# Kernel optimization log

Hardware: AMD Instinct MI355X
Metric: run time of the kernel (lower is better)

The kernel has to match this reference:

```python
import jax, jax.numpy as jnp
import numpy as np

N = 50000      # nodes
E = 600000     # directed edges (before self-loops)
IN, HID, OUT = 512, 128, 40
EPS_BN = 1e-5
DROP_P = 0.5   # hardcoded in forward via BernoulliDropout(0.5)

# BinActive: sign() forward, straight-through estimator backward (|x|<=1 gate)
@jax.custom_vjp
def binactive(x):
    return jnp.sign(x)

def _ba_fwd(x):
    return jnp.sign(x), x

def _ba_bwd(x, g):
    return (g * (jnp.abs(x) <= 1.0).astype(g.dtype),)

binactive.defvjp(_ba_fwd, _ba_bwd)


def setup_inputs() -> dict:
    key = jax.random.key(0)
    ks = jax.random.split(key, 8)
    x = jax.random.normal(ks[0], (N, IN), dtype=jnp.float32)
    edge_index = jax.random.randint(ks[1], (2, E), 0, N, dtype=jnp.int64)
    w0 = jax.random.normal(ks[2], (IN, HID), dtype=jnp.float32) * 0.05
    b0 = jnp.zeros((HID,), jnp.float32)
    w1 = jax.random.normal(ks[3], (HID, HID), dtype=jnp.float32) * 0.05
    b1 = jnp.zeros((HID,), jnp.float32)
    w2 = jax.random.normal(ks[4], (HID, OUT), dtype=jnp.float32) * 0.05
    b2 = jnp.zeros((OUT,), jnp.float32)
    return {"x": x, "edge_index": edge_index,
            "w0": w0, "b0": b0, "w1": w1, "b1": b1, "w2": w2, "b2": b2}


def _gcn_norm(edge_index):
    # add self-loops, compute symmetric normalization deg^-1/2 A deg^-1/2
    loops = jnp.arange(N, dtype=edge_index.dtype)
    row = jnp.concatenate([edge_index[0], loops])  # destinations
    col = jnp.concatenate([edge_index[1], loops])  # sources
    deg = jax.ops.segment_sum(jnp.ones_like(row, dtype=jnp.float32), row, num_segments=N)
    dinv = jnp.where(deg > 0, deg ** -0.5, 0.0)
    norm = dinv[row] * dinv[col]                   # [E+N]
    return row, col, norm


def _gcn_conv(x, w, b, row, col, norm):
    # binarized weight: sign(w) scaled by mean(|w|) (XNOR-style)
    wb = binactive(w) * jnp.mean(jnp.abs(w))
    h = x @ wb                                     # [N, out]
    msg = h[col] * norm[:, None]                   # gather + scale
    agg = jax.ops.segment_sum(msg, row, num_segments=N)
    return agg + b


def reference(x, edge_index, w0, b0, w1, b1, w2, b2):
    # BatchNorm1d(affine=False), training-mode batch stats over nodes
    mean = jnp.mean(x, axis=0)
    var = jnp.var(x, axis=0)
    h = (x - mean) / jnp.sqrt(var + EPS_BN)

    row, col, norm = _gcn_norm(edge_index)
    dkey = jax.random.key(42)
    weights = [(w0, b0), (w1, b1), (w2, b2)]
    n_layers = len(weights)
    for i, (w, b) in enumerate(weights):
        h = binactive(h)
        h = _gcn_conv(h, w, b, row, col, norm)
        if i != n_layers - 1:  # BernoulliDropout(0.5)
            mask = jax.random.bernoulli(jax.random.fold_in(dkey, i), 1.0 - DROP_P, h.shape)
            h = h * mask.astype(h.dtype) * (1.0 / (1.0 - DROP_P))
    return jax.nn.log_softmax(h, axis=1)
```

## Files before the change

kernel.cpp:

```cpp
#include <hip/hip_runtime.h>
#include <stdint.h>
#include <stddef.h>

#define NN 50000
#define NE 600000
#define DI 512
#define DH 128
#define DO 40
#define MTOT (NN * DH)
#define NBLK ((NN + 255) / 256)

using int4v = __attribute__((ext_vector_type(4))) int;

__host__ __device__ inline uint32_t rotl32(uint32_t v, int d) {
  return (v << d) | (v >> (32 - d));
}

__host__ __device__ inline void threefry2x32(uint32_t k0, uint32_t k1,
                                             uint32_t c0, uint32_t c1,
                                             uint32_t* o0, uint32_t* o1) {
  uint32_t ks0 = k0, ks1 = k1, ks2 = k0 ^ k1 ^ 0x1BD11BDAu;
  uint32_t x0 = c0 + ks0, x1 = c1 + ks1;
  const int R0[4] = {13, 15, 26, 6};
  const int R1[4] = {17, 29, 16, 24};
#define TF_R4(R) { x0 += x1; x1 = rotl32(x1, R[0]); x1 ^= x0; \
                   x0 += x1; x1 = rotl32(x1, R[1]); x1 ^= x0; \
                   x0 += x1; x1 = rotl32(x1, R[2]); x1 ^= x0; \
                   x0 += x1; x1 = rotl32(x1, R[3]); x1 ^= x0; }
  TF_R4(R0); x0 += ks1; x1 += ks2 + 1u;
  TF_R4(R1); x0 += ks2; x1 += ks0 + 2u;
  TF_R4(R0); x0 += ks0; x1 += ks1 + 3u;
  TF_R4(R1); x0 += ks1; x1 += ks2 + 4u;
  TF_R4(R0); x0 += ks2; x1 += ks0 + 5u;
#undef TF_R4
  *o0 = x0; *o1 = x1;
}

__global__ void colsum_kernel(const float* __restrict__ x,
                              double* __restrict__ colsum) {
  int t = threadIdx.x;
  int r0 = blockIdx.x * 250;
  double s0 = 0.0, s1 = 0.0;
  for (int r = r0; r < r0 + 250; r += 10) {
    double v0[10], v1[10];
#pragma unroll
    for (int u = 0; u < 10; ++u) {
      v0[u] = (double)x[(size_t)(r + u) * DI + t];
      v1[u] = (double)x[(size_t)(r + u) * DI + t + 256];
    }
#pragma unroll
    for (int u = 0; u < 10; ++u) {
      s0 += v0[u];
      s1 += v1[u];
    }
  }
  unsafeAtomicAdd(&colsum[t], s0);
  unsafeAtomicAdd(&colsum[t + 256], s1);
}

__global__ void mean_finalize(double* __restrict__ colsum) {
  int c = blockIdx.x * blockDim.x + threadIdx.x;
  if (c < DI) colsum[c] = colsum[c] / (double)NN;
}

__device__ inline void wfuse_body(const float* __restrict__ w,
                                  uint32_t* __restrict__ frag,
                                  double* __restrict__ slot,
                                  int K, int C, int NT, int blk,
                                  double* red) {
  int steps = K >> 6;
  int total = steps * NT * 64 * 4;
  int idx = blk * 256 + threadIdx.x;
  double a = 0.0;
  if (idx < total) {
    int dw = idx & 3;
    int lane = (idx >> 2) & 63;
    int rest = idx >> 8;
    int t = rest % NT;
    int s = rest / NT;
    int n = t * 16 + (lane & 15);
    int kbase = s * 64 + (lane >> 4) * 16 + dw * 4;
    uint32_t v = 0;
    if (n < C) {
#pragma unroll
      for (int j = 0; j < 4; ++j) {
        float wv = w[(size_t)(kbase + j) * C + n];
        uint32_t sg = (uint8_t)(int8_t)((wv > 0.f) ? 1 : ((wv < 0.f) ? -1 : 0));
        v |= sg << (8 * j);
        a += (double)fabsf(wv);
      }
    }
    frag[idx] = v;
  }
  red[threadIdx.x] = a;
  __syncthreads();
  for (int ofs = 128; ofs > 0; ofs >>= 1) {
    if (threadIdx.x < ofs) red[threadIdx.x] += red[threadIdx.x + ofs];
    __syncthreads();
  }
  if (threadIdx.x == 0) unsafeAtomicAdd(slot, red[0]);
}

__global__ void wfuse_all(const float* __restrict__ w0,
                          const float* __restrict__ w1,
                          const float* __restrict__ w2,
                          uint32_t* __restrict__ f0,
                          uint32_t* __restrict__ f1,
                          uint32_t* __restrict__ f2,
                          double* __restrict__ slots) {
  __shared__ double red[256];
  int b = blockIdx.x;
  if (b < 64)       wfuse_body(w0, f0, slots + 0, DI, DH, 8, b,      red);
  else if (b < 80)  wfuse_body(w1, f1, slots + 1, DH, DH, 8, b - 64, red);
  else              wfuse_body(w2, f2, slots + 2, DH, DO, 3, b - 80, red);
}

__global__ void deg_edges(const int* __restrict__ ei, uint32_t* __restrict__ deg) {
  int e = blockIdx.x * blockDim.x + threadIdx.x;
  if (e < NE) atomicAdd(&deg[ei[e]], 1u);
}

__global__ void scan_blocks(const uint32_t* __restrict__ deg,
                            uint32_t* __restrict__ rowptr,
                            uint32_t* __restrict__ bsum,
                            double* __restrict__ dinv) {
  __shared__ uint32_t bs[256];
  int t = threadIdx.x;
  int i = blockIdx.x * 256 + t;
  uint32_t v = (i < NN) ? deg[i] : 0u;
  if (i < NN) dinv[i] = 1.0 / sqrt((double)(v + 1u));
  bs[t] = v;
  __syncthreads();
  for (int ofs = 1; ofs < 256; ofs <<= 1) {
    uint32_t add = (t >= ofs) ? bs[t - ofs] : 0u;
    __syncthreads();
    bs[t] += add;
    __syncthreads();
  }
  if (i < NN) rowptr[i] = bs[t] - v;
  if (t == 255) bsum[blockIdx.x] = bs[255];
}

__global__ void scan_bsum(const uint32_t* __restrict__ bsum,
                          uint32_t* __restrict__ base) {
  __shared__ uint32_t bs[256];
  int t = threadIdx.x;
  uint32_t v = (t < NBLK) ? bsum[t] : 0u;
  bs[t] = v;
  __syncthreads();
  for (int ofs = 1; ofs < 256; ofs <<= 1) {
    uint32_t add = (t >= ofs) ? bs[t - ofs] : 0u;
    __syncthreads();
    bs[t] += add;
    __syncthreads();
  }
  if (t < NBLK) base[t] = bs[t] - v;
}

__global__ void scan_addbase(uint32_t* __restrict__ rowptr,
                             const uint32_t* __restrict__ base) {
  int i = blockIdx.x * 256 + threadIdx.x;
  if (i < NN) rowptr[i] += base[blockIdx.x];
  if (i == 0) rowptr[NN] = NE;
}

__global__ void csr_fill(const int* __restrict__ ei,
                         const uint32_t* __restrict__ rowptr,
                         uint32_t* __restrict__ cursor,
                         int* __restrict__ csr_src) {
  int e = blockIdx.x * blockDim.x + threadIdx.x;
  if (e >= NE) return;
  int dst = ei[e], src = ei[NE + e];
  uint32_t pos = rowptr[dst] + atomicAdd(&cursor[dst], 1u);
  csr_src[pos] = src;
}

template <int STEPS, int NT, int C, int SHIFT>
__global__ void gemm_mfma(const int8_t* __restrict__ S,
                          const uint32_t* __restrict__ frag,
                          int8_t* __restrict__ H) {
  extern __shared__ uint4 lb[];
  const int tot = STEPS * NT * 64;
  const uint4* fg = (const uint4*)frag;
  for (int i = threadIdx.x; i < tot; i += 256) lb[i] = fg[i];
  __syncthreads();
  const int lane = threadIdx.x & 63;
  const int wv = threadIdx.x >> 6;
  const int r0 = (blockIdx.x * 4 + wv) * 16;
  if (r0 >= NN) return;
  const int m = lane & 15, q = lane >> 4;
  const int K = STEPS * 64;
  const int8_t* sp = S + (size_t)(r0 + m) * K + q * 16;
  int4v acc[NT];
#pragma unroll
  for (int t = 0; t < NT; ++t) acc[t] = (int4v){0, 0, 0, 0};
#pragma unroll
  for (int s = 0; s < STEPS; ++s) {
    int4v a = *(const int4v*)(sp + (size_t)s * 64);
#pragma unroll
    for (int t = 0; t < NT; ++t) {
      int4v b = *(const int4v*)&lb[(s * NT + t) * 64 + lane];
      acc[t] = __builtin_amdgcn_mfma_i32_16x16x64_i8(a, b, acc[t], 0, 0, 0);
    }
  }
  int8_t* hp = H + (size_t)r0 * C;
#pragma unroll
  for (int t = 0; t < NT; ++t) {
    int n = t * 16 + m;
    if (n < C) {
#pragma unroll
      for (int r = 0; r < 4; ++r)
        hp[(size_t)(q * 4 + r) * C + n] = (int8_t)(acc[t][r] >> SHIFT);
    }
  }
}

__global__ void gemm0_fused(const float* __restrict__ x,
                            const double* __restrict__ mean,
                            const uint32_t* __restrict__ frag,
                            int8_t* __restrict__ H) {
  extern __shared__ uint4 lb[];
  const int tot = 8 * 8 * 64;
  const uint4* fg = (const uint4*)frag;
  for (int i = threadIdx.x; i < tot; i += 256) lb[i] = fg[i];
  __syncthreads();
  const int lane = threadIdx.x & 63;
  const int wv = threadIdx.x >> 6;
  const int r0 = (blockIdx.x * 4 + wv) * 16;
  if (r0 >= NN) return;
  const int m = lane & 15, q = lane >> 4;
  const float* xp = x + (size_t)(r0 + m) * DI + q * 16;
  const double* mp0 = mean + q * 16;
  int4v acc[8];
#pragma unroll
  for (int t = 0; t < 8; ++t) acc[t] = (int4v){0, 0, 0, 0};
#pragma unroll
  for (int s = 0; s < 8; ++s) {
    const float* xs = xp + s * 64;
    const double* mp = mp0 + s * 64;
    int4v a;
#pragma unroll
    for (int w4 = 0; w4 < 4; ++w4) {
      float4 f = *(const float4*)(xs + 4 * w4);
      double v0 = (double)f.x - mp[4 * w4 + 0];
      double v1 = (double)f.y - mp[4 * w4 + 1];
      double v2 = (double)f.z - mp[4 * w4 + 2];
      double v3 = (double)f.w - mp[4 * w4 + 3];
      uint32_t o = 0;
      o |= (uint8_t)(int8_t)((v0 > 0.0) ? 1 : ((v0 < 0.0) ? -1 : 0));
      o |= ((uint32_t)(uint8_t)(int8_t)((v1 > 0.0) ? 1 : ((v1 < 0.0) ? -1 : 0))) << 8;
      o |= ((uint32_t)(uint8_t)(int8_t)((v2 > 0.0) ? 1 : ((v2 < 0.0) ? -1 : 0))) << 16;
      o |= ((uint32_t)(uint8_t)(int8_t)((v3 > 0.0) ? 1 : ((v3 < 0.0) ? -1 : 0))) << 24;
      a[w4] = (int)o;
    }
#pragma unroll
    for (int t = 0; t < 8; ++t) {
      int4v b = *(const int4v*)&lb[(s * 8 + t) * 64 + lane];
      acc[t] = __builtin_amdgcn_mfma_i32_16x16x64_i8(a, b, acc[t], 0, 0, 0);
    }
  }
  int8_t* hp = H + (size_t)r0 * DH;
#pragma unroll
  for (int t = 0; t < 8; ++t) {
    int n = t * 16 + m;
#pragma unroll
    for (int r = 0; r < 4; ++r)
      hp[(size_t)(q * 4 + r) * DH + n] = (int8_t)(acc[t][r] >> 1);
  }
}

__global__ void gather128(const uint32_t* __restrict__ rowptr,
                          const int* __restrict__ csr_src,
                          const double* __restrict__ dinv,
                          const int8_t* __restrict__ H,
                          const float* __restrict__ b,
                          int8_t* __restrict__ Sout,
                          const double* __restrict__ wsum, double cnt,
                          uint32_t fk0, uint32_t fk1) {
  int d = (int)(((size_t)blockIdx.x * blockDim.x + threadIdx.x) >> 6);
  int lane = threadIdx.x & 63;
  if (d >= NN) return;
  const int g = lane >> 5, p = lane & 31;
  double a0 = 0.0, a1 = 0.0, a2 = 0.0, a3 = 0.0;
  const uint32_t e0 = rowptr[d];
  const int L = (int)(rowptr[d + 1] - e0) + 1;
  for (int c0 = 0; c0 < L; c0 += 64) {
    const int n = min(64, L - c0);
    const int my = c0 + lane;
    int sidx = d;
    if (my > 0 && my < L) sidx = csr_src[e0 + my - 1];
    double wv = dinv[sidx];
    int t = 0;
    {
      int sA = 0, sB = 0; double wA = 0.0, wB = 0.0;
      uint32_t hA = 0, hB = 0;
      if (4 <= n) {
        sA = __shfl(sidx, g);      wA = __shfl(wv, g);
        sB = __shfl(sidx, 2 + g);  wB = __shfl(wv, 2 + g);
        hA = *(const uint32_t*)(H + (size_t)sA * DH + 4 * p);
        hB = *(const uint32_t*)(H + (size_t)sB * DH + 4 * p);
      }
      for (; t + 4 <= n; t += 4) {
        const uint32_t cA = hA, cB = hB;
        const double vA = wA, vB = wB;
        if (t + 8 <= n) {
          sA = __shfl(sidx, t + 4 + g);  wA = __shfl(wv, t + 4 + g);
          sB = __shfl(sidx, t + 6 + g);  wB = __shfl(wv, t + 6 + g);
          hA = *(const uint32_t*)(H + (size_t)sA * DH + 4 * p);
          hB = *(const uint32_t*)(H + (size_t)sB * DH + 4 * p);
        }
        a0 += vA * (double)(int8_t)(cA);
        a1 += vA * (double)(int8_t)(cA >> 8);
        a2 += vA * (double)(int8_t)(cA >> 16);
        a3 += vA * (double)(int8_t)(cA >> 24);
        a0 += vB * (double)(int8_t)(cB);
        a1 += vB * (double)(int8_t)(cB >> 8);
        a2 += vB * (double)(int8_t)(cB >> 16);
        a3 += vB * (double)(int8_t)(cB >> 24);
      }
    }
    for (; t < n; t += 2) {
      const int j = t + g;
      const bool on = (j < n);
      const int jc = on ? j : 0;
      int s = __shfl(sidx, jc);
      double w = __shfl(wv, jc);
      w = on ? w : 0.0;
      uint32_t hv = *(const uint32_t*)(H + (size_t)s * DH + 4 * p);
      a0 += w * (double)(int8_t)(hv);
      a1 += w * (double)(int8_t)(hv >> 8);
      a2 += w * (double)(int8_t)(hv >> 16);
      a3 += w * (double)(int8_t)(hv >> 24);
    }
  }
  a0 += __shfl_xor(a0, 32);
  a1 += __shfl_xor(a1, 32);
  a2 += __shfl_xor(a2, 32);
  a3 += __shfl_xor(a3, 32);
  double sc = (wsum[0] / cnt) * dinv[d];
  int ch = 4 * p + 2 * g;
  int j0 = d * DH + ch;
  double va = sc * ((g == 0) ? a0 : a2) + (double)b[ch];
  double vb = sc * ((g == 0) ? a1 : a3) + (double)b[ch + 1];
  int s0 = (va > 0.0) ? 1 : ((va < 0.0) ? -1 : 0);
  int s1 = (vb > 0.0) ? 1 : ((vb < 0.0) ? -1 : 0);
  uint32_t r0, r1, bits0, bits1;
  threefry2x32(fk0, fk1, 0u, (uint32_t)j0, &r0, &r1);
  bits0 = r0 ^ r1;
  threefry2x32(fk0, fk1, 0u, (uint32_t)(j0 + 1), &r0, &r1);
  bits1 = r0 ^ r1;
  float u0 = __uint_as_float((bits0 >> 9) | 0x3f800000u) - 1.0f;
  float u1 = __uint_as_float((bits1 >> 9) | 0x3f800000u) - 1.0f;
  uint8_t o0 = (u0 < 0.5f) ? (uint8_t)(int8_t)s0 : (uint8_t)0;
  uint8_t o1 = (u1 < 0.5f) ? (uint8_t)(int8_t)s1 : (uint8_t)0;
  *(uint16_t*)(Sout + j0) = (uint16_t)(o0 | ((uint16_t)o1 << 8));
}

__global__ void gather40_lsm(const uint32_t* __restrict__ rowptr,
                             const int* __restrict__ csr_src,
                             const double* __restrict__ dinv,
                             const int8_t* __restrict__ H,
                             const float* __restrict__ b2,
                             const double* __restrict__ wsum,
                             float* __restrict__ out) {
  int d = (int)(((size_t)blockIdx.x * blockDim.x + threadIdx.x) >> 6);
  int lane = threadIdx.x & 63;
  if (d >= NN) return;
  const int g = lane >> 5, p = lane & 31;
  const bool act = (p < 20);
  double a0 = 0.0, a1 = 0.0;
  const uint32_t e0 = rowptr[d];
  const int L = (int)(rowptr[d + 1] - e0) + 1;
  for (int c0 = 0; c0 < L; c0 += 64) {
    const int n = min(64, L - c0);
    const int my = c0 + lane;
    int sidx = d;
    if (my > 0 && my < L) sidx = csr_src[e0 + my - 1];
    double wv = dinv[sidx];
    int t = 0;
    {
      int sA = 0, sB = 0; double wA = 0.0, wB = 0.0;
      uint16_t hA = 0, hB = 0;
      if (4 <= n) {
        sA = __shfl(sidx, g);      wA = __shfl(wv, g);
        sB = __shfl(sidx, 2 + g);  wB = __shfl(wv, 2 + g);
        if (act) {
          hA = *(const uint16_t*)(H + (size_t)sA * DO + 2 * p);
          hB = *(const uint16_t*)(H + (size_t)sB * DO + 2 * p);
        }
      }
      for (; t + 4 <= n; t += 4) {
        const uint16_t cA = hA, cB = hB;
        const double vA = wA, vB = wB;
        if (t + 8 <= n) {
          sA = __shfl(sidx, t + 4 + g);  wA = __shfl(wv, t + 4 + g);
          sB = __shfl(sidx, t + 6 + g);  wB = __shfl(wv, t + 6 + g);
          if (act) {
            hA = *(const uint16_t*)(H + (size_t)sA * DO + 2 * p);
            hB = *(const uint16_t*)(H + (size_t)sB * DO + 2 * p);
          }
        }
        if (act) {
          a0 += vA * (double)(int8_t)(cA);
          a1 += vA * (double)(int8_t)(cA >> 8);
          a0 += vB * (double)(int8_t)(cB);
          a1 += vB * (double)(int8_t)(cB >> 8);
        }
      }
    }
    for (; t < n; t += 2) {
      const int j = t + g;
      const bool on = (j < n);
      const int jc = on ? j : 0;
      int s = __shfl(sidx, jc);
      double w = __shfl(wv, jc);
      w = on ? w : 0.0;
      if (act) {
        uint16_t hv = *(const uint16_t*)(H + (size_t)s * DO + 2 * p);
        a0 += w * (double)(int8_t)(hv);
        a1 += w * (double)(int8_t)(hv >> 8);
      }
    }
  }
  a0 += __shfl_xor(a0, 32);
  a1 += __shfl_xor(a1, 32);
  double sc = (wsum[0] / (double)(DH * DO)) * dinv[d];
  const bool lead = (g == 0) && act;
  double v0 = 0.0, v1 = 0.0;
  if (act) {
    v0 = sc * a0 + (double)b2[2 * p];
    v1 = sc * a1 + (double)b2[2 * p + 1];
  }
  double mx = lead ? fmax(v0, v1) : -1.0e300;
  for (int ofs = 32; ofs > 0; ofs >>= 1) mx = fmax(mx, __shfl_xor(mx, ofs));
  float ex = lead ? (expf((float)(v0 - mx)) + expf((float)(v1 - mx))) : 0.f;
  for (int ofs = 32; ofs > 0; ofs >>= 1) ex += __shfl_xor(ex, ofs);
  float l = logf(ex);
  if (lead) {
    float2 o = make_float2((float)(v0 - mx) - l, (float)(v1 - mx) - l);
    *(float2*)(out + (size_t)d * DO + 2 * p) = o;
  }
}

extern "C" void kernel_launch(void* const* d_in, const int* in_sizes, int n_in,
                              void* d_out, int out_size, void* d_ws, size_t ws_size,
                              hipStream_t stream) {
  (void)in_sizes; (void)n_in; (void)out_size; (void)ws_size;
  const float* x  = (const float*)d_in[0];
  const int*   ei = (const int*)d_in[1];
  const float* w0 = (const float*)d_in[2];
  const float* b0 = (const float*)d_in[3];
  const float* w1 = (const float*)d_in[4];
  const float* b1 = (const float*)d_in[5];
  const float* w2 = (const float*)d_in[6];
  const float* b2 = (const float*)d_in[7];
  float* out = (float*)d_out;

  char* wsb = (char*)d_ws;
  double*   mean_d = (double*)wsb;
  double*   wsum_d = (double*)(wsb + 4096);
  uint32_t* deg_e  = (uint32_t*)(wsb + 4224);
  uint32_t* cursor = (uint32_t*)(wsb + 204224);
  size_t cur = 404480;
  uint32_t* rowptr = (uint32_t*)(wsb + cur); cur += 200064;
  double*   dinv_d = (double*)(wsb + cur);  cur += 400000;
  cur = (cur + 255) & ~255ull;
  uint32_t* bsum = (uint32_t*)(wsb + cur); cur += 1024;
  uint32_t* base = (uint32_t*)(wsb + cur); cur += 1024;
  int*    csr_src = (int*)(wsb + cur);    cur += (size_t)NE * 4;
  cur = (cur + 255) & ~255ull;
  uint32_t* FR0 = (uint32_t*)(wsb + cur); cur += 8 * 8 * 64 * 16;
  uint32_t* FR1 = (uint32_t*)(wsb + cur); cur += 2 * 8 * 64 * 16;
  uint32_t* FR2 = (uint32_t*)(wsb + cur); cur += 2 * 3 * 64 * 16;
  int8_t* S1  = (int8_t*)(wsb + cur); cur += (size_t)MTOT;
  cur = (cur + 255) & ~255ull;
  int8_t* H8 = (int8_t*)(wsb + cur); cur += (size_t)MTOT;

  uint32_t fkA0, fkA1, fkB0, fkB1;
  threefry2x32(0u, 42u, 0u, 0u, &fkA0, &fkA1);
  threefry2x32(0u, 42u, 0u, 1u, &fkB0, &fkB1);

  hipMemsetAsync(wsb, 0, 404224, stream);

  colsum_kernel<<<200, 256, 0, stream>>>(x, mean_d);
  mean_finalize<<<2, 256, 0, stream>>>(mean_d);
  wfuse_all<<<86, 256, 0, stream>>>(w0, w1, w2, FR0, FR1, FR2, wsum_d);
  deg_edges<<<(NE + 255) / 256, 256, 0, stream>>>(ei, deg_e);
  scan_blocks<<<NBLK, 256, 0, stream>>>(deg_e, rowptr, bsum, dinv_d);
  scan_bsum<<<1, 256, 0, stream>>>(bsum, base);
  scan_addbase<<<NBLK, 256, 0, stream>>>(rowptr, base);
  csr_fill<<<(NE + 255) / 256, 256, 0, stream>>>(ei, rowptr, cursor, csr_src);

  const int gemm_blocks = (NN / 16 + 3) / 4;
  const int node_blocks = (NN * 64) / 256 + 1;
  const size_t sh0 = 8 * 8 * 64 * 16;
  const size_t sh1 = 2 * 8 * 64 * 16;
  const size_t sh2 = 2 * 3 * 64 * 16;

  gemm0_fused<<<gemm_blocks, 256, sh0, stream>>>(x, mean_d, FR0, H8);
  gather128<<<node_blocks, 256, 0, stream>>>(rowptr, csr_src, dinv_d, H8, b0, S1,
                                             wsum_d + 0, (double)(DI * DH / 2),
                                             fkA0, fkA1);

  gemm_mfma<2, 8, DH, 0><<<gemm_blocks, 256, sh1, stream>>>(S1, FR1, H8);
  gather128<<<node_blocks, 256, 0, stream>>>(rowptr, csr_src, dinv_d, H8, b1, S1,
                                             wsum_d + 1, (double)(DH * DH),
                                             fkB0, fkB1);

  gemm_mfma<2, 3, DO, 0><<<gemm_blocks, 256, sh2, stream>>>(S1, FR2, H8);
  gather40_lsm<<<node_blocks, 256, 0, stream>>>(rowptr, csr_src, dinv_d, H8, b2,
                                                wsum_d + 2, out);
}
```

Baseline: 401.4 us.

## Fuse prologue kernels and fold scan base offset into consumers

Merges colsum, degree counting and weight packing into one prologue launch, folds the mean division into the block-scan kernel, and removes the scan_addbase pass by having csr_fill and the gather kernels add the per-block base offset themselves. This cuts the launch count from roughly 12 to 8 and drops one pass over rowptr. In exchange, every gather adds an extra base lookup per node, and the end offset now takes a branch instead of reading rowptr[NN].

```diff
diff --git a/kernel.cpp b/kernel.cpp
--- a/kernel.cpp
+++ b/kernel.cpp
@@ -9,6 +9,7 @@
 #define DO 40
 #define MTOT (NN * DH)
 #define NBLK ((NN + 255) / 256)
+#define DEGB ((NE + 255) / 256)
 
 using int4v = __attribute__((ext_vector_type(4))) int;
 
@@ -36,10 +37,10 @@
   *o0 = x0; *o1 = x1;
 }
 
-__global__ void colsum_kernel(const float* __restrict__ x,
-                              double* __restrict__ colsum) {
+__device__ inline void colsum_body(const float* __restrict__ x,
+                                   double* __restrict__ colsum, int blk) {
   int t = threadIdx.x;
-  int r0 = blockIdx.x * 250;
+  int r0 = blk * 250;
   double s0 = 0.0, s1 = 0.0;
   for (int r = r0; r < r0 + 250; r += 10) {
     double v0[10], v1[10];
@@ -56,11 +57,6 @@
   }
   unsafeAtomicAdd(&colsum[t], s0);
   unsafeAtomicAdd(&colsum[t + 256], s1);
-}
-
-__global__ void mean_finalize(double* __restrict__ colsum) {
-  int c = blockIdx.x * blockDim.x + threadIdx.x;
-  if (c < DI) colsum[c] = colsum[c] / (double)NN;
 }
 
 __device__ inline void wfuse_body(const float* __restrict__ w,
@@ -101,44 +97,58 @@
   if (threadIdx.x == 0) unsafeAtomicAdd(slot, red[0]);
 }
 
-__global__ void wfuse_all(const float* __restrict__ w0,
-                          const float* __restrict__ w1,
-                          const float* __restrict__ w2,
-                          uint32_t* __restrict__ f0,
-                          uint32_t* __restrict__ f1,
-                          uint32_t* __restrict__ f2,
-                          double* __restrict__ slots) {
+__global__ void prologue_fused(const float* __restrict__ x,
+                               double* __restrict__ colsum,
+                               const int* __restrict__ ei,
+                               uint32_t* __restrict__ deg,
+                               const float* __restrict__ w0,
+                               const float* __restrict__ w1,
+                               const float* __restrict__ w2,
+                               uint32_t* __restrict__ f0,
+                               uint32_t* __restrict__ f1,
+                               uint32_t* __restrict__ f2,
+                               double* __restrict__ slots) {
   __shared__ double red[256];
   int b = blockIdx.x;
-  if (b < 64)       wfuse_body(w0, f0, slots + 0, DI, DH, 8, b,      red);
-  else if (b < 80)  wfuse_body(w1, f1, slots + 1, DH, DH, 8, b - 64, red);
-  else              wfuse_body(w2, f2, slots + 2, DH, DO, 3, b - 80, red);
-}
-
-__global__ void deg_edges(const int* __restrict__ ei, uint32_t* __restrict__ deg) {
-  int e = blockIdx.x * blockDim.x + threadIdx.x;
-  if (e < NE) atomicAdd(&deg[ei[e]], 1u);
-}
-
-__global__ void scan_blocks(const uint32_t* __restrict__ deg,
-                            uint32_t* __restrict__ rowptr,
-                            uint32_t* __restrict__ bsum,
-                            double* __restrict__ dinv) {
+  if (b < 200) {
+    colsum_body(x, colsum, b);
+  } else if (b < 200 + DEGB) {
+    int e = (b - 200) * 256 + threadIdx.x;
+    if (e < NE) atomicAdd(&deg[ei[e]], 1u);
+  } else {
+    int wb = b - (200 + DEGB);
+    if (wb < 64)       wfuse_body(w0, f0, slots + 0, DI, DH, 8, wb,      red);
+    else if (wb < 80)  wfuse_body(w1, f1, slots + 1, DH, DH, 8, wb - 64, red);
+    else               wfuse_body(w2, f2, slots + 2, DH, DO, 3, wb - 80, red);
+  }
+}
+
+__global__ void scan_mean(const uint32_t* __restrict__ deg,
+                          uint32_t* __restrict__ rowptr,
+                          uint32_t* __restrict__ bsum,
+                          double* __restrict__ dinv,
+                          double* __restrict__ colsum) {
   __shared__ uint32_t bs[256];
+  int b = blockIdx.x;
   int t = threadIdx.x;
-  int i = blockIdx.x * 256 + t;
-  uint32_t v = (i < NN) ? deg[i] : 0u;
-  if (i < NN) dinv[i] = 1.0 / sqrt((double)(v + 1u));
-  bs[t] = v;
-  __syncthreads();
-  for (int ofs = 1; ofs < 256; ofs <<= 1) {
-    uint32_t add = (t >= ofs) ? bs[t - ofs] : 0u;
+  if (b < NBLK) {
+    int i = b * 256 + t;
+    uint32_t v = (i < NN) ? deg[i] : 0u;
+    if (i < NN) dinv[i] = 1.0 / sqrt((double)(v + 1u));
+    bs[t] = v;
     __syncthreads();
-    bs[t] += add;
-    __syncthreads();
-  }
-  if (i < NN) rowptr[i] = bs[t] - v;
-  if (t == 255) bsum[blockIdx.x] = bs[255];
+    for (int ofs = 1; ofs < 256; ofs <<= 1) {
+      uint32_t add = (t >= ofs) ? bs[t - ofs] : 0u;
+      __syncthreads();
+      bs[t] += add;
+      __syncthreads();
+    }
+    if (i < NN) rowptr[i] = bs[t] - v;
+    if (t == 255) bsum[b] = bs[255];
+  } else {
+    int c = (b - NBLK) * 256 + t;
+    if (c < DI) colsum[c] = colsum[c] / (double)NN;
+  }
 }
 
 __global__ void scan_bsum(const uint32_t* __restrict__ bsum,
@@ -157,21 +167,15 @@
   if (t < NBLK) base[t] = bs[t] - v;
 }
 
-__global__ void scan_addbase(uint32_t* __restrict__ rowptr,
-                             const uint32_t* __restrict__ base) {
-  int i = blockIdx.x * 256 + threadIdx.x;
-  if (i < NN) rowptr[i] += base[blockIdx.x];
-  if (i == 0) rowptr[NN] = NE;
-}
-
 __global__ void csr_fill(const int* __restrict__ ei,
                          const uint32_t* __restrict__ rowptr,
+                         const uint32_t* __restrict__ base,
                          uint32_t* __restrict__ cursor,
                          int* __restrict__ csr_src) {
   int e = blockIdx.x * blockDim.x + threadIdx.x;
   if (e >= NE) return;
   int dst = ei[e], src = ei[NE + e];
-  uint32_t pos = rowptr[dst] + atomicAdd(&cursor[dst], 1u);
+  uint32_t pos = rowptr[dst] + base[dst >> 8] + atomicAdd(&cursor[dst], 1u);
   csr_src[pos] = src;
 }
 
@@ -270,6 +274,7 @@
 }
 
 __global__ void gather128(const uint32_t* __restrict__ rowptr,
+                          const uint32_t* __restrict__ base,
                           const int* __restrict__ csr_src,
                           const double* __restrict__ dinv,
                           const int8_t* __restrict__ H,
@@ -282,8 +287,9 @@
   if (d >= NN) return;
   const int g = lane >> 5, p = lane & 31;
   double a0 = 0.0, a1 = 0.0, a2 = 0.0, a3 = 0.0;
-  const uint32_t e0 = rowptr[d];
-  const int L = (int)(rowptr[d + 1] - e0) + 1;
+  const uint32_t e0 = rowptr[d] + base[d >> 8];
+  const uint32_t e1 = (d + 1 < NN) ? (rowptr[d + 1] + base[(d + 1) >> 8]) : NE;
+  const int L = (int)(e1 - e0) + 1;
   for (int c0 = 0; c0 < L; c0 += 64) {
     const int n = min(64, L - c0);
     const int my = c0 + lane;
@@ -357,6 +363,7 @@
 }
 
 __global__ void gather40_lsm(const uint32_t* __restrict__ rowptr,
+                             const uint32_t* __restrict__ base,
                              const int* __restrict__ csr_src,
                              const double* __restrict__ dinv,
                              const int8_t* __restrict__ H,
@@ -369,8 +376,9 @@
   const int g = lane >> 5, p = lane & 31;
   const bool act = (p < 20);
   double a0 = 0.0, a1 = 0.0;
-  const uint32_t e0 = rowptr[d];
-  const int L = (int)(rowptr[d + 1] - e0) + 1;
+  const uint32_t e0 = rowptr[d] + base[d >> 8];
+  const uint32_t e1 = (d + 1 < NN) ? (rowptr[d + 1] + base[(d + 1) >> 8]) : NE;
+  const int L = (int)(e1 - e0) + 1;
   for (int c0 = 0; c0 < L; c0 += 64) {
     const int n = min(64, L - c0);
     const int my = c0 + lane;
@@ -482,14 +490,11 @@
 
   hipMemsetAsync(wsb, 0, 404224, stream);
 
-  colsum_kernel<<<200, 256, 0, stream>>>(x, mean_d);
-  mean_finalize<<<2, 256, 0, stream>>>(mean_d);
-  wfuse_all<<<86, 256, 0, stream>>>(w0, w1, w2, FR0, FR1, FR2, wsum_d);
-  deg_edges<<<(NE + 255) / 256, 256, 0, stream>>>(ei, deg_e);
-  scan_blocks<<<NBLK, 256, 0, stream>>>(deg_e, rowptr, bsum, dinv_d);
+  prologue_fused<<<200 + DEGB + 86, 256, 0, stream>>>(
+      x, mean_d, ei, deg_e, w0, w1, w2, FR0, FR1, FR2, wsum_d);
+  scan_mean<<<NBLK + 2, 256, 0, stream>>>(deg_e, rowptr, bsum, dinv_d, mean_d);
   scan_bsum<<<1, 256, 0, stream>>>(bsum, base);
-  scan_addbase<<<NBLK, 256, 0, stream>>>(rowptr, base);
-  csr_fill<<<(NE + 255) / 256, 256, 0, stream>>>(ei, rowptr, cursor, csr_src);
+  csr_fill<<<DEGB, 256, 0, stream>>>(ei, rowptr, base, cursor, csr_src);
 
   const int gemm_blocks = (NN / 16 + 3) / 4;
   const int node_blocks = (NN * 64) / 256 + 1;
@@ -498,16 +503,16 @@
   const size_t sh2 = 2 * 3 * 64 * 16;
 
   gemm0_fused<<<gemm_blocks, 256, sh0, stream>>>(x, mean_d, FR0, H8);
-  gather128<<<node_blocks, 256, 0, stream>>>(rowptr, csr_src, dinv_d, H8, b0, S1,
-                                             wsum_d + 0, (double)(DI * DH / 2),
-                                             fkA0, fkA1);
+  gather128<<<node_blocks, 256, 0, stream>>>(rowptr, base, csr_src, dinv_d, H8,
+                                             b0, S1, wsum_d + 0,
+                                             (double)(DI * DH / 2), fkA0, fkA1);
 
   gemm_mfma<2, 8, DH, 0><<<gemm_blocks, 256, sh1, stream>>>(S1, FR1, H8);
-  gather128<<<node_blocks, 256, 0, stream>>>(rowptr, csr_src, dinv_d, H8, b1, S1,
-                                             wsum_d + 1, (double)(DH * DH),
-                                             fkB0, fkB1);
+  gather128<<<node_blocks, 256, 0, stream>>>(rowptr, base, csr_src, dinv_d, H8,
+                                             b1, S1, wsum_d + 1,
+                                             (double)(DH * DH), fkB0, fkB1);
 
   gemm_mfma<2, 3, DO, 0><<<gemm_blocks, 256, sh2, stream>>>(S1, FR2, H8);
-  gather40_lsm<<<node_blocks, 256, 0, stream>>>(rowptr, csr_src, dinv_d, H8, b2,
-                                                wsum_d + 2, out);
-}
+  gather40_lsm<<<node_blocks, 256, 0, stream>>>(rowptr, base, csr_src, dinv_d,
+                                                H8, b2, wsum_d + 2, out);
+}
```

Result: faster. 388.1 us (-3.3%).
